# Optimization experiments

Measured on AMD Instinct MI355X. Metric: run time of the kernel, lower is better.

## Reference

```python
import jax, jax.numpy as jnp
import numpy as np

D_MODEL = 1024
NUM_HEADS = 4
EXPAND_K = 1.0
EXPAND_V = 2.0
KEY_DIM = int(D_MODEL * EXPAND_K)      # 1024
VALUE_DIM = int(D_MODEL * EXPAND_V)    # 2048
HEAD_K = KEY_DIM // NUM_HEADS          # 256
HEAD_V = VALUE_DIM // NUM_HEADS        # 512
CHUNK = 64
EPS = 1e-5
ROPE_BASE = 10000.0


def setup_inputs() -> dict:
    key = jax.random.key(0)
    ks = jax.random.split(key, 7)
    B, T = 4, 2048
    s = 0.02
    return {
        "x": jax.random.normal(ks[0], (B, T, D_MODEL), dtype=jnp.float32),
        "Wq": jax.random.normal(ks[1], (KEY_DIM, D_MODEL), dtype=jnp.float32) * s,
        "Wk": jax.random.normal(ks[2], (KEY_DIM, D_MODEL), dtype=jnp.float32) * s,
        "Wv": jax.random.normal(ks[3], (VALUE_DIM, D_MODEL), dtype=jnp.float32) * s,
        "Wg": jax.random.normal(ks[4], (VALUE_DIM, D_MODEL), dtype=jnp.float32) * s,
        "Wo": jax.random.normal(ks[5], (D_MODEL, VALUE_DIM), dtype=jnp.float32) * s,
        "gnorm_w": jnp.ones((HEAD_V,), dtype=jnp.float32),
    }


def _apply_rotary(q, k):
    # q,k: [B,T,H,dk]; NeoX-style (non-interleaved) rotary on full head dim
    d = q.shape[-1]
    half = d // 2
    inv_freq = 1.0 / (ROPE_BASE ** (jnp.arange(0, d, 2, dtype=jnp.float32) / d))
    t = jnp.arange(q.shape[1], dtype=jnp.float32)
    freqs = t[:, None] * inv_freq[None, :]          # [T, d/2]
    cos = jnp.cos(freqs)[None, :, None, :]
    sin = jnp.sin(freqs)[None, :, None, :]

    def rot(x):
        x1, x2 = x[..., :half], x[..., half:]
        return jnp.concatenate([x1 * cos - x2 * sin, x2 * cos + x1 * sin], axis=-1)

    return rot(q), rot(k)


def _chunk_retention(q, k, v, gamma):
    # q,k: [B,T,H,dk]; v: [B,T,H,dv]; gamma: [H] per-head decay
    B, T, H, dk = q.shape
    dv = v.shape[-1]
    C = CHUNK
    N = T // C
    qc = q.reshape(B, N, C, H, dk).transpose(1, 0, 3, 2, 4)  # [N,B,H,C,dk]
    kc = k.reshape(B, N, C, H, dk).transpose(1, 0, 3, 2, 4)
    vc = v.reshape(B, N, C, H, dv).transpose(1, 0, 3, 2, 4)  # [N,B,H,C,dv]

    i = jnp.arange(C, dtype=jnp.float32)
    cross_dec = gamma[:, None] ** (i + 1.0)          # [H,C] gamma^{i+1}: query decay vs incoming state
    k_dec = gamma[:, None] ** (C - 1.0 - i)          # [H,C] key decay toward chunk end
    diff = i[:, None] - i[None, :]                   # [C,C]
    mask = jnp.where(diff >= 0, gamma[:, None, None] ** diff, 0.0)  # [H,C,C]
    gC = gamma ** C                                  # [H]

    def step(S, inp):
        # S: [B,H,dk,dv]
        qb, kb, vb = inp
        attn = jnp.einsum('bhid,bhjd->bhij', qb, kb) * mask
        o_intra = jnp.einsum('bhij,bhjv->bhiv', attn, vb)
        o_inter = jnp.einsum('bhid,bhdv->bhiv', qb * cross_dec[:, :, None], S)
        S_new = gC[:, None, None] * S + jnp.einsum('bhjd,bhjv->bhdv', kb * k_dec[:, :, None], vb)
        return S_new, o_intra + o_inter

    S0 = jnp.zeros((B, H, dk, dv), dtype=q.dtype)
    _, o = jax.lax.scan(step, S0, (qc, kc, vc))      # o: [N,B,H,C,dv]
    return o.transpose(1, 0, 3, 2, 4).reshape(B, T, H, dv)


def reference(x, Wq, Wk, Wv, Wg, Wo, gnorm_w):
    B, T, _ = x.shape
    H = NUM_HEADS
    q = (x @ Wq.T).reshape(B, T, H, HEAD_K)
    k = (x @ Wk.T).reshape(B, T, H, HEAD_K)
    v = (x @ Wv.T).reshape(B, T, H, HEAD_V)
    g = (x @ Wg.T).reshape(B, T, H, HEAD_V)

    q, k = _apply_rotary(q, k)
    q = q * (HEAD_K ** -0.5)

    # fixed multi-scale decays: gamma_h = 1 - 2^{-5-h}
    gamma = 1.0 - jnp.exp2(-5.0 - jnp.arange(H, dtype=jnp.float32))

    o = _chunk_retention(q, k, v, gamma)             # [B,T,H,dv]

    # per-head RMSNorm + swish gate, then output projection
    var = jnp.mean(o * o, axis=-1, keepdims=True)
    o = o * jax.lax.rsqrt(var + EPS) * gnorm_w
    o = o * (g * jax.nn.sigmoid(g))
    return o.reshape(B, T, H * HEAD_V) @ Wo.T
```

## Files before the change

kernel.cpp:

```cpp
#include <hip/hip_runtime.h>
#include <cstdint>
#include <cstddef>

#define T_SEQ 2048
#define DM    1024
#define HK    256
#define HV    512
#define NH    4
#define KDIM  1024
#define VDIM  2048

typedef __attribute__((ext_vector_type(8))) short bf16x8;
typedef __attribute__((ext_vector_type(4))) float f32x4;
#define AS1 __attribute__((address_space(1)))
#define AS3 __attribute__((address_space(3)))

static __device__ inline unsigned short f2bf(float f) {
  unsigned u = __float_as_uint(f);
  unsigned rnd = 0x7fffu + ((u >> 16) & 1u);
  return (unsigned short)((u + rnd) >> 16);
}
static __device__ inline float bf2f(unsigned short h) {
  unsigned u = ((unsigned)h) << 16;
  return __uint_as_float(u);
}

__global__ __launch_bounds__(256) void cast_split(const float* __restrict__ in,
                                                  unsigned short* __restrict__ hi,
                                                  unsigned short* __restrict__ lo,
                                                  int n4) {
  int i = blockIdx.x * 256 + threadIdx.x;
  if (i >= n4) return;
  float4 v = ((const float4*)in)[i];
  ushort4 h, l;
  h.x = f2bf(v.x); l.x = f2bf(v.x - bf2f(h.x));
  h.y = f2bf(v.y); l.y = f2bf(v.y - bf2f(h.y));
  h.z = f2bf(v.z); l.z = f2bf(v.z - bf2f(h.z));
  h.w = f2bf(v.w); l.w = f2bf(v.w - bf2f(h.w));
  ((ushort4*)hi)[i] = h;
  ((ushort4*)lo)[i] = l;
}

__global__ __launch_bounds__(256) void gemm_bf16s(const unsigned short* __restrict__ Ah,
                                                  const unsigned short* __restrict__ Al,
                                                  const unsigned short* __restrict__ Wh,
                                                  const unsigned short* __restrict__ Wl,
                                                  float* __restrict__ C,
                                                  int M, int N, int K) {
  __shared__ unsigned short AhS[128 * 32];
  __shared__ unsigned short AlS[128 * 32];
  __shared__ unsigned short WhS[128 * 32];
  __shared__ unsigned short WlS[128 * 32];
  const int t = threadIdx.x;
  const int l = t & 63;
  const int w = t >> 6;
  const int bm = blockIdx.y * 128;
  const int bn = blockIdx.x * 128;
  const int wm = (w >> 1) * 64;
  const int wn = (w & 1) * 64;

  f32x4 acc[4][4];
#pragma unroll
  for (int i = 0; i < 4; ++i)
#pragma unroll
    for (int j = 0; j < 4; ++j)
#pragma unroll
      for (int r = 0; r < 4; ++r) acc[i][j][r] = 0.f;

  const int srow = w * 32 + (l >> 2);
  const int scol = (l & 3) * 8;
  const size_t gOffA = (size_t)(bm + srow) * K + scol;
  const size_t gOffW = (size_t)(bn + srow) * K + scol;
  const size_t rowStep = (size_t)16 * K;
  unsigned short* lAh0 = &AhS[(w * 32) * 32];
  unsigned short* lAh1 = &AhS[(w * 32 + 16) * 32];
  unsigned short* lAl0 = &AlS[(w * 32) * 32];
  unsigned short* lAl1 = &AlS[(w * 32 + 16) * 32];
  unsigned short* lWh0 = &WhS[(w * 32) * 32];
  unsigned short* lWh1 = &WhS[(w * 32 + 16) * 32];
  unsigned short* lWl0 = &WlS[(w * 32) * 32];
  unsigned short* lWl1 = &WlS[(w * 32 + 16) * 32];

  for (int k0 = 0; k0 < K; k0 += 32) {
    __syncthreads();
    __builtin_amdgcn_global_load_lds((const AS1 void*)(Ah + gOffA + k0),           (AS3 void*)lAh0, 16, 0, 0);
    __builtin_amdgcn_global_load_lds((const AS1 void*)(Ah + gOffA + rowStep + k0), (AS3 void*)lAh1, 16, 0, 0);
    __builtin_amdgcn_global_load_lds((const AS1 void*)(Al + gOffA + k0),           (AS3 void*)lAl0, 16, 0, 0);
    __builtin_amdgcn_global_load_lds((const AS1 void*)(Al + gOffA + rowStep + k0), (AS3 void*)lAl1, 16, 0, 0);
    __builtin_amdgcn_global_load_lds((const AS1 void*)(Wh + gOffW + k0),           (AS3 void*)lWh0, 16, 0, 0);
    __builtin_amdgcn_global_load_lds((const AS1 void*)(Wh + gOffW + rowStep + k0), (AS3 void*)lWh1, 16, 0, 0);
    __builtin_amdgcn_global_load_lds((const AS1 void*)(Wl + gOffW + k0),           (AS3 void*)lWl0, 16, 0, 0);
    __builtin_amdgcn_global_load_lds((const AS1 void*)(Wl + gOffW + rowStep + k0), (AS3 void*)lWl1, 16, 0, 0);
    __syncthreads();

    bf16x8 ah[4], al[4], bh[4], bl[4];
#pragma unroll
    for (int i = 0; i < 4; ++i) {
      int aoff = (wm + i * 16 + (l & 15)) * 32 + (l >> 4) * 8;
      int boff = (wn + i * 16 + (l & 15)) * 32 + (l >> 4) * 8;
      ah[i] = *(const bf16x8*)&AhS[aoff];
      al[i] = *(const bf16x8*)&AlS[aoff];
      bh[i] = *(const bf16x8*)&WhS[boff];
      bl[i] = *(const bf16x8*)&WlS[boff];
    }
#pragma unroll
    for (int i = 0; i < 4; ++i)
#pragma unroll
      for (int j = 0; j < 4; ++j) {
        acc[i][j] = __builtin_amdgcn_mfma_f32_16x16x32_bf16(ah[i], bh[j], acc[i][j], 0, 0, 0);
        acc[i][j] = __builtin_amdgcn_mfma_f32_16x16x32_bf16(ah[i], bl[j], acc[i][j], 0, 0, 0);
        acc[i][j] = __builtin_amdgcn_mfma_f32_16x16x32_bf16(al[i], bh[j], acc[i][j], 0, 0, 0);
      }
  }

  const int cr = (l >> 4) * 4;
  const int cc = l & 15;
#pragma unroll
  for (int i = 0; i < 4; ++i)
#pragma unroll
    for (int j = 0; j < 4; ++j)
#pragma unroll
      for (int r = 0; r < 4; ++r)
        C[(size_t)(bm + wm + i * 16 + cr + r) * N + (bn + wn + j * 16 + cc)] = acc[i][j][r];
}

__global__ __launch_bounds__(256) void rope_kernel(float* __restrict__ q,
                                                   float* __restrict__ k) {
  int idx = blockIdx.x * 256 + threadIdx.x;
  int f  = idx & 127;
  int h  = (idx >> 7) & 3;
  int tt = (idx >> 9) & 2047;
  int b  = idx >> 20;
  size_t a0 = ((size_t)(b * T_SEQ + tt)) * KDIM + h * HK + f;
  size_t a1 = a0 + 128;
  float invf = powf(10000.0f, -(float)f * (1.0f / 128.0f));
  float ang  = (float)tt * invf;
  float s, c;
  sincosf(ang, &s, &c);
  float q1 = q[a0], q2 = q[a1];
  q[a0] = (q1 * c - q2 * s) * 0.0625f;
  q[a1] = (q2 * c + q1 * s) * 0.0625f;
  float k1 = k[a0], k2 = k[a1];
  k[a0] = k1 * c - k2 * s;
  k[a1] = k2 * c + k1 * s;
}

__global__ __launch_bounds__(256) void retn_intra(const float* __restrict__ q,
                                                  const float* __restrict__ k,
                                                  const float* __restrict__ v,
                                                  float* __restrict__ o) {
  const int n = blockIdx.x, h = blockIdx.y, b = blockIdx.z;
  const int t = threadIdx.x;
  const int t0 = n * 64;
  __shared__ float gpow[65];
  __shared__ __align__(16) float qS[64][68];
  __shared__ __align__(16) float kS[64][68];
  __shared__ __align__(16) float attnS[64][68];
  if (t <= 64) {
    float gamma = 1.0f - exp2f(-5.0f - (float)h);
    gpow[t] = powf(gamma, (float)t);
  }
  const size_t baseQK = (size_t)(b * T_SEQ + t0) * KDIM + h * HK;
  const size_t baseV  = (size_t)(b * T_SEQ + t0) * VDIM + h * HV;
  const int i0 = (t >> 4) * 4;
  const int j0 = (t & 15) * 4;
  float acc[4][4] = {};
  for (int s = 0; s < 4; ++s) {
    __syncthreads();
    __builtin_amdgcn_sched_barrier(0);
#pragma unroll
    for (int r = 0; r < 4; ++r) {
      int idx = t + 256 * r;
      int row = idx >> 4, c4 = (idx & 15) * 4;
      *(float4*)&qS[row][c4] = *(const float4*)&q[baseQK + (size_t)row * KDIM + s * 64 + c4];
      *(float4*)&kS[row][c4] = *(const float4*)&k[baseQK + (size_t)row * KDIM + s * 64 + c4];
    }
    __syncthreads();
    __builtin_amdgcn_sched_barrier(0);
    for (int d = 0; d < 64; d += 4) {
      float4 a0 = *(const float4*)&qS[i0 + 0][d];
      float4 a1 = *(const float4*)&qS[i0 + 1][d];
      float4 a2 = *(const float4*)&qS[i0 + 2][d];
      float4 a3 = *(const float4*)&qS[i0 + 3][d];
      float4 b0 = *(const float4*)&kS[j0 + 0][d];
      float4 b1 = *(const float4*)&kS[j0 + 1][d];
      float4 b2 = *(const float4*)&kS[j0 + 2][d];
      float4 b3 = *(const float4*)&kS[j0 + 3][d];
      acc[0][0]=fmaf(a0.x,b0.x,acc[0][0]); acc[0][0]=fmaf(a0.y,b0.y,acc[0][0]); acc[0][0]=fmaf(a0.z,b0.z,acc[0][0]); acc[0][0]=fmaf(a0.w,b0.w,acc[0][0]);
      acc[0][1]=fmaf(a0.x,b1.x,acc[0][1]); acc[0][1]=fmaf(a0.y,b1.y,acc[0][1]); acc[0][1]=fmaf(a0.z,b1.z,acc[0][1]); acc[0][1]=fmaf(a0.w,b1.w,acc[0][1]);
      acc[0][2]=fmaf(a0.x,b2.x,acc[0][2]); acc[0][2]=fmaf(a0.y,b2.y,acc[0][2]); acc[0][2]=fmaf(a0.z,b2.z,acc[0][2]); acc[0][2]=fmaf(a0.w,b2.w,acc[0][2]);
      acc[0][3]=fmaf(a0.x,b3.x,acc[0][3]); acc[0][3]=fmaf(a0.y,b3.y,acc[0][3]); acc[0][3]=fmaf(a0.z,b3.z,acc[0][3]); acc[0][3]=fmaf(a0.w,b3.w,acc[0][3]);
      acc[1][0]=fmaf(a1.x,b0.x,acc[1][0]); acc[1][0]=fmaf(a1.y,b0.y,acc[1][0]); acc[1][0]=fmaf(a1.z,b0.z,acc[1][0]); acc[1][0]=fmaf(a1.w,b0.w,acc[1][0]);
      acc[1][1]=fmaf(a1.x,b1.x,acc[1][1]); acc[1][1]=fmaf(a1.y,b1.y,acc[1][1]); acc[1][1]=fmaf(a1.z,b1.z,acc[1][1]); acc[1][1]=fmaf(a1.w,b1.w,acc[1][1]);
      acc[1][2]=fmaf(a1.x,b2.x,acc[1][2]); acc[1][2]=fmaf(a1.y,b2.y,acc[1][2]); acc[1][2]=fmaf(a1.z,b2.z,acc[1][2]); acc[1][2]=fmaf(a1.w,b2.w,acc[1][2]);
      acc[1][3]=fmaf(a1.x,b3.x,acc[1][3]); acc[1][3]=fmaf(a1.y,b3.y,acc[1][3]); acc[1][3]=fmaf(a1.z,b3.z,acc[1][3]); acc[1][3]=fmaf(a1.w,b3.w,acc[1][3]);
      acc[2][0]=fmaf(a2.x,b0.x,acc[2][0]); acc[2][0]=fmaf(a2.y,b0.y,acc[2][0]); acc[2][0]=fmaf(a2.z,b0.z,acc[2][0]); acc[2][0]=fmaf(a2.w,b0.w,acc[2][0]);
      acc[2][1]=fmaf(a2.x,b1.x,acc[2][1]); acc[2][1]=fmaf(a2.y,b1.y,acc[2][1]); acc[2][1]=fmaf(a2.z,b1.z,acc[2][1]); acc[2][1]=fmaf(a2.w,b1.w,acc[2][1]);
      acc[2][2]=fmaf(a2.x,b2.x,acc[2][2]); acc[2][2]=fmaf(a2.y,b2.y,acc[2][2]); acc[2][2]=fmaf(a2.z,b2.z,acc[2][2]); acc[2][2]=fmaf(a2.w,b2.w,acc[2][2]);
      acc[2][3]=fmaf(a2.x,b3.x,acc[2][3]); acc[2][3]=fmaf(a2.y,b3.y,acc[2][3]); acc[2][3]=fmaf(a2.z,b3.z,acc[2][3]); acc[2][3]=fmaf(a2.w,b3.w,acc[2][3]);
      acc[3][0]=fmaf(a3.x,b0.x,acc[3][0]); acc[3][0]=fmaf(a3.y,b0.y,acc[3][0]); acc[3][0]=fmaf(a3.z,b0.z,acc[3][0]); acc[3][0]=fmaf(a3.w,b0.w,acc[3][0]);
      acc[3][1]=fmaf(a3.x,b1.x,acc[3][1]); acc[3][1]=fmaf(a3.y,b1.y,acc[3][1]); acc[3][1]=fmaf(a3.z,b1.z,acc[3][1]); acc[3][1]=fmaf(a3.w,b1.w,acc[3][1]);
      acc[3][2]=fmaf(a3.x,b2.x,acc[3][2]); acc[3][2]=fmaf(a3.y,b2.y,acc[3][2]); acc[3][2]=fmaf(a3.z,b2.z,acc[3][2]); acc[3][2]=fmaf(a3.w,b2.w,acc[3][2]);
      acc[3][3]=fmaf(a3.x,b3.x,acc[3][3]); acc[3][3]=fmaf(a3.y,b3.y,acc[3][3]); acc[3][3]=fmaf(a3.z,b3.z,acc[3][3]); acc[3][3]=fmaf(a3.w,b3.w,acc[3][3]);
    }
  }
  __syncthreads();
#pragma unroll
  for (int ii = 0; ii < 4; ++ii)
#pragma unroll
    for (int jj = 0; jj < 4; ++jj) {
      int i = i0 + ii, j = j0 + jj;
      attnS[i][j] = (i >= j) ? acc[ii][jj] * gpow[i - j] : 0.0f;
    }
  float (*vS)[68] = qS;
  for (int vb = 0; vb < 8; ++vb) {
    __syncthreads();
    __builtin_amdgcn_sched_barrier(0);
#pragma unroll
    for (int r = 0; r < 4; ++r) {
      int idx = t + 256 * r;
      int row = idx >> 4, c4 = (idx & 15) * 4;
      *(float4*)&vS[row][c4] = *(const float4*)&v[baseV + (size_t)row * VDIM + vb * 64 + c4];
    }
    __syncthreads();
    __builtin_amdgcn_sched_barrier(0);
    float oa[4][4] = {};
    for (int j = 0; j < 64; j += 4) {
      float4 p0 = *(const float4*)&attnS[i0 + 0][j];
      float4 p1 = *(const float4*)&attnS[i0 + 1][j];
      float4 p2 = *(const float4*)&attnS[i0 + 2][j];
      float4 p3 = *(const float4*)&attnS[i0 + 3][j];
      float4 v0 = *(const float4*)&vS[j + 0][j0];
      float4 v1 = *(const float4*)&vS[j + 1][j0];
      float4 v2 = *(const float4*)&vS[j + 2][j0];
      float4 v3 = *(const float4*)&vS[j + 3][j0];
      oa[0][0]=fmaf(p0.x,v0.x,oa[0][0]); oa[0][0]=fmaf(p0.y,v1.x,oa[0][0]); oa[0][0]=fmaf(p0.z,v2.x,oa[0][0]); oa[0][0]=fmaf(p0.w,v3.x,oa[0][0]);
      oa[0][1]=fmaf(p0.x,v0.y,oa[0][1]); oa[0][1]=fmaf(p0.y,v1.y,oa[0][1]); oa[0][1]=fmaf(p0.z,v2.y,oa[0][1]); oa[0][1]=fmaf(p0.w,v3.y,oa[0][1]);
      oa[0][2]=fmaf(p0.x,v0.z,oa[0][2]); oa[0][2]=fmaf(p0.y,v1.z,oa[0][2]); oa[0][2]=fmaf(p0.z,v2.z,oa[0][2]); oa[0][2]=fmaf(p0.w,v3.z,oa[0][2]);
      oa[0][3]=fmaf(p0.x,v0.w,oa[0][3]); oa[0][3]=fmaf(p0.y,v1.w,oa[0][3]); oa[0][3]=fmaf(p0.z,v2.w,oa[0][3]); oa[0][3]=fmaf(p0.w,v3.w,oa[0][3]);
      oa[1][0]=fmaf(p1.x,v0.x,oa[1][0]); oa[1][0]=fmaf(p1.y,v1.x,oa[1][0]); oa[1][0]=fmaf(p1.z,v2.x,oa[1][0]); oa[1][0]=fmaf(p1.w,v3.x,oa[1][0]);
      oa[1][1]=fmaf(p1.x,v0.y,oa[1][1]); oa[1][1]=fmaf(p1.y,v1.y,oa[1][1]); oa[1][1]=fmaf(p1.z,v2.y,oa[1][1]); oa[1][1]=fmaf(p1.w,v3.y,oa[1][1]);
      oa[1][2]=fmaf(p1.x,v0.z,oa[1][2]); oa[1][2]=fmaf(p1.y,v1.z,oa[1][2]); oa[1][2]=fmaf(p1.z,v2.z,oa[1][2]); oa[1][2]=fmaf(p1.w,v3.z,oa[1][2]);
      oa[1][3]=fmaf(p1.x,v0.w,oa[1][3]); oa[1][3]=fmaf(p1.y,v1.w,oa[1][3]); oa[1][3]=fmaf(p1.z,v2.w,oa[1][3]); oa[1][3]=fmaf(p1.w,v3.w,oa[1][3]);
      oa[2][0]=fmaf(p2.x,v0.x,oa[2][0]); oa[2][0]=fmaf(p2.y,v1.x,oa[2][0]); oa[2][0]=fmaf(p2.z,v2.x,oa[2][0]); oa[2][0]=fmaf(p2.w,v3.x,oa[2][0]);
      oa[2][1]=fmaf(p2.x,v0.y,oa[2][1]); oa[2][1]=fmaf(p2.y,v1.y,oa[2][1]); oa[2][1]=fmaf(p2.z,v2.y,oa[2][1]); oa[2][1]=fmaf(p2.w,v3.y,oa[2][1]);
      oa[2][2]=fmaf(p2.x,v0.z,oa[2][2]); oa[2][2]=fmaf(p2.y,v1.z,oa[2][2]); oa[2][2]=fmaf(p2.z,v2.z,oa[2][2]); oa[2][2]=fmaf(p2.w,v3.z,oa[2][2]);
      oa[2][3]=fmaf(p2.x,v0.w,oa[2][3]); oa[2][3]=fmaf(p2.y,v1.w,oa[2][3]); oa[2][3]=fmaf(p2.z,v2.w,oa[2][3]); oa[2][3]=fmaf(p2.w,v3.w,oa[2][3]);
      oa[3][0]=fmaf(p3.x,v0.x,oa[3][0]); oa[3][0]=fmaf(p3.y,v1.x,oa[3][0]); oa[3][0]=fmaf(p3.z,v2.x,oa[3][0]); oa[3][0]=fmaf(p3.w,v3.x,oa[3][0]);
      oa[3][1]=fmaf(p3.x,v0.y,oa[3][1]); oa[3][1]=fmaf(p3.y,v1.y,oa[3][1]); oa[3][1]=fmaf(p3.z,v2.y,oa[3][1]); oa[3][1]=fmaf(p3.w,v3.y,oa[3][1]);
      oa[3][2]=fmaf(p3.x,v0.z,oa[3][2]); oa[3][2]=fmaf(p3.y,v1.z,oa[3][2]); oa[3][2]=fmaf(p3.z,v2.z,oa[3][2]); oa[3][2]=fmaf(p3.w,v3.z,oa[3][2]);
      oa[3][3]=fmaf(p3.x,v0.w,oa[3][3]); oa[3][3]=fmaf(p3.y,v1.w,oa[3][3]); oa[3][3]=fmaf(p3.z,v2.w,oa[3][3]); oa[3][3]=fmaf(p3.w,v3.w,oa[3][3]);
    }
#pragma unroll
    for (int ii = 0; ii < 4; ++ii)
      *(float4*)&o[baseV + (size_t)(i0 + ii) * VDIM + vb * 64 + j0] =
          make_float4(oa[ii][0], oa[ii][1], oa[ii][2], oa[ii][3]);
  }
}


__global__ __launch_bounds__(256) void retn_gstate(const float* __restrict__ k,
                                                   const float* __restrict__ v,
                                                   float* __restrict__ Tbuf) {
  const int bh = blockIdx.x; const int b = bh >> 2, h = bh & 3;
  const int g = blockIdx.y;
  const int dkt = blockIdx.z >> 3, dvt = blockIdx.z & 7;
  const int t = threadIdx.x;
  __shared__ float gpow[65];
  __shared__ __align__(16) float kS[64][68];
  __shared__ __align__(16) float vS[64][68];
  if (t <= 64) gpow[t] = powf(1.0f - exp2f(-5.0f - (float)h), (float)t);
  __syncthreads();
  const float gC = gpow[64];
  const size_t baseK = (size_t)(b * T_SEQ + g * 512) * KDIM + h * HK + dkt * 64;
  const size_t baseV = (size_t)(b * T_SEQ + g * 512) * VDIM + h * HV + dvt * 64;
  const int dk0 = (t & 15) * 4, c0 = (t >> 4) * 4;
  float S[4][4] = {};
  for (int c = 0; c < 8; ++c) {
    const int t0 = c * 64;
    __syncthreads();
    __builtin_amdgcn_sched_barrier(0);
#pragma unroll
    for (int r = 0; r < 4; ++r) {
      int idx = t + 256 * r; int row = idx >> 4, c4 = (idx & 15) * 4;
      float4 kv = *(const float4*)&k[baseK + (size_t)(t0 + row) * KDIM + c4];
      float kd = gpow[63 - row];
      kv.x *= kd; kv.y *= kd; kv.z *= kd; kv.w *= kd;
      *(float4*)&kS[row][c4] = kv;
      *(float4*)&vS[row][c4] = *(const float4*)&v[baseV + (size_t)(t0 + row) * VDIM + c4];
    }
    __syncthreads();
    __builtin_amdgcn_sched_barrier(0);
#pragma unroll
    for (int ii = 0; ii < 4; ++ii)
#pragma unroll
      for (int jj = 0; jj < 4; ++jj) S[ii][jj] *= gC;
    for (int j = 0; j < 64; ++j) {
      float4 kv = *(const float4*)&kS[j][dk0];
      float4 vv = *(const float4*)&vS[j][c0];
      S[0][0] = fmaf(kv.x, vv.x, S[0][0]); S[0][1] = fmaf(kv.x, vv.y, S[0][1]);
      S[0][2] = fmaf(kv.x, vv.z, S[0][2]); S[0][3] = fmaf(kv.x, vv.w, S[0][3]);
      S[1][0] = fmaf(kv.y, vv.x, S[1][0]); S[1][1] = fmaf(kv.y, vv.y, S[1][1]);
      S[1][2] = fmaf(kv.y, vv.z, S[1][2]); S[1][3] = fmaf(kv.y, vv.w, S[1][3]);
      S[2][0] = fmaf(kv.z, vv.x, S[2][0]); S[2][1] = fmaf(kv.z, vv.y, S[2][1]);
      S[2][2] = fmaf(kv.z, vv.z, S[2][2]); S[2][3] = fmaf(kv.z, vv.w, S[2][3]);
      S[3][0] = fmaf(kv.w, vv.x, S[3][0]); S[3][1] = fmaf(kv.w, vv.y, S[3][1]);
      S[3][2] = fmaf(kv.w, vv.z, S[3][2]); S[3][3] = fmaf(kv.w, vv.w, S[3][3]);
    }
  }
  const size_t tb = (((size_t)g * 16 + bh) * 256 + dkt * 64 + dk0) * 512 + (size_t)dvt * 64 + c0;
#pragma unroll
  for (int ii = 0; ii < 4; ++ii)
    *(float4*)&Tbuf[tb + (size_t)ii * 512] = make_float4(S[ii][0], S[ii][1], S[ii][2], S[ii][3]);
}

__global__ __launch_bounds__(256) void retn_scan(float* __restrict__ Tbuf) {
  int i = blockIdx.x * 256 + threadIdx.x;
  int h = (i >> 15) & 3;
  float gamma = 1.0f - exp2f(-5.0f - (float)h);
  float gG = powf(gamma, 512.0f);
  float4* T = (float4*)Tbuf;
  const int slab = 524288;
  float4 t0 = T[i], t1 = T[i + slab], t2 = T[i + 2 * slab];
  float4 s2, s3;
  s2.x = fmaf(gG, t0.x, t1.x); s2.y = fmaf(gG, t0.y, t1.y);
  s2.z = fmaf(gG, t0.z, t1.z); s2.w = fmaf(gG, t0.w, t1.w);
  s3.x = fmaf(gG, s2.x, t2.x); s3.y = fmaf(gG, s2.y, t2.y);
  s3.z = fmaf(gG, s2.z, t2.z); s3.w = fmaf(gG, s2.w, t2.w);
  T[i + slab] = s2; T[i + 2 * slab] = s3;
}

__global__ __launch_bounds__(256) void retn_inter2(const float* __restrict__ q,
                                                   const float* __restrict__ k,
                                                   const float* __restrict__ v,
                                                   float* __restrict__ o,
                                                   const float* __restrict__ Sbuf) {
  const int bh = blockIdx.x; const int b = bh >> 2, h = bh & 3;
  const int g = blockIdx.y;
  const int dvt = blockIdx.z;
  const int t = threadIdx.x;
  __shared__ float gpow[65];
  __shared__ __align__(16) float qS[64][68];
  __shared__ __align__(16) float kS[64][68];
  __shared__ __align__(16) float sS[64][68];
  __shared__ __align__(16) float vS[64][68];
  if (t <= 64) gpow[t] = powf(1.0f - exp2f(-5.0f - (float)h), (float)t);
  __syncthreads();
  const float gC = gpow[64];
  const int rq = (t & 15) * 4;
  const int c0 = (t >> 4) * 4;
  const int i0 = (t >> 4) * 4;
  const int v0 = (t & 15) * 4;
  const size_t baseQK = (size_t)(b * T_SEQ + g * 512) * KDIM + h * HK;
  const size_t baseV  = (size_t)(b * T_SEQ + g * 512) * VDIM + h * HV + (size_t)dvt * 64;

  float S[4][4][4];
  if (g > 0) {
    const size_t sb = (((size_t)(g - 1) * 16 + bh) * 256) * 512 + (size_t)dvt * 64 + c0;
#pragma unroll
    for (int b4 = 0; b4 < 4; ++b4)
#pragma unroll
      for (int i = 0; i < 4; ++i) {
        float4 tmp = *(const float4*)&Sbuf[sb + (size_t)(b4 * 64 + rq + i) * 512];
        S[b4][i][0] = tmp.x; S[b4][i][1] = tmp.y; S[b4][i][2] = tmp.z; S[b4][i][3] = tmp.w;
      }
  } else {
#pragma unroll
    for (int b4 = 0; b4 < 4; ++b4)
#pragma unroll
      for (int i = 0; i < 4; ++i) {
        S[b4][i][0] = 0.f; S[b4][i][1] = 0.f; S[b4][i][2] = 0.f; S[b4][i][3] = 0.f;
      }
  }

  for (int c = 0; c < 8; ++c) {
    const int t0 = c * 64;
    __syncthreads();
    __builtin_amdgcn_sched_barrier(0);
#pragma unroll
    for (int r = 0; r < 4; ++r) {
      int idx = t + 256 * r; int row = idx >> 4, c4 = (idx & 15) * 4;
      *(float4*)&vS[row][c4] = *(const float4*)&v[baseV + (size_t)(t0 + row) * VDIM + c4];
    }
    float oa[4][4] = {};
#pragma unroll
    for (int b4 = 0; b4 < 4; ++b4) {
      __syncthreads();
      __builtin_amdgcn_sched_barrier(0);
#pragma unroll
      for (int i = 0; i < 4; ++i)
        *(float4*)&sS[rq + i][c0] =
            make_float4(S[b4][i][0], S[b4][i][1], S[b4][i][2], S[b4][i][3]);
#pragma unroll
      for (int r = 0; r < 4; ++r) {
        int idx = t + 256 * r; int row = idx >> 4, c4 = (idx & 15) * 4;
        float4 qv = *(const float4*)&q[baseQK + (size_t)(t0 + row) * KDIM + b4 * 64 + c4];
        float gp = gpow[row + 1];
        qv.x *= gp; qv.y *= gp; qv.z *= gp; qv.w *= gp;
        *(float4*)&qS[row][c4] = qv;
      }
#pragma unroll
      for (int r = 0; r < 4; ++r) {
        int idx = t + 256 * r; int row = idx >> 4, c4 = (idx & 15) * 4;
        float4 kv = *(const float4*)&k[baseQK + (size_t)(t0 + row) * KDIM + b4 * 64 + c4];
        float kd = gpow[63 - row];
        kv.x *= kd; kv.y *= kd; kv.z *= kd; kv.w *= kd;
        *(float4*)&kS[row][c4] = kv;
      }
      __syncthreads();
      __builtin_amdgcn_sched_barrier(0);
      for (int d = 0; d < 64; d += 4) {
        float4 a0 = *(const float4*)&qS[i0 + 0][d];
        float4 a1 = *(const float4*)&qS[i0 + 1][d];
        float4 a2 = *(const float4*)&qS[i0 + 2][d];
        float4 a3 = *(const float4*)&qS[i0 + 3][d];
        float4 s0 = *(const float4*)&sS[d + 0][v0];
        float4 s1 = *(const float4*)&sS[d + 1][v0];
        float4 s2 = *(const float4*)&sS[d + 2][v0];
        float4 s3 = *(const float4*)&sS[d + 3][v0];
        oa[0][0]=fmaf(a0.x,s0.x,oa[0][0]); oa[0][0]=fmaf(a0.y,s1.x,oa[0][0]); oa[0][0]=fmaf(a0.z,s2.x,oa[0][0]); oa[0][0]=fmaf(a0.w,s3.x,oa[0][0]);
        oa[0][1]=fmaf(a0.x,s0.y,oa[0][1]); oa[0][1]=fmaf(a0.y,s1.y,oa[0][1]); oa[0][1]=fmaf(a0.z,s2.y,oa[0][1]); oa[0][1]=fmaf(a0.w,s3.y,oa[0][1]);
        oa[0][2]=fmaf(a0.x,s0.z,oa[0][2]); oa[0][2]=fmaf(a0.y,s1.z,oa[0][2]); oa[0][2]=fmaf(a0.z,s2.z,oa[0][2]); oa[0][2]=fmaf(a0.w,s3.z,oa[0][2]);
        oa[0][3]=fmaf(a0.x,s0.w,oa[0][3]); oa[0][3]=fmaf(a0.y,s1.w,oa[0][3]); oa[0][3]=fmaf(a0.z,s2.w,oa[0][3]); oa[0][3]=fmaf(a0.w,s3.w,oa[0][3]);
        oa[1][0]=fmaf(a1.x,s0.x,oa[1][0]); oa[1][0]=fmaf(a1.y,s1.x,oa[1][0]); oa[1][0]=fmaf(a1.z,s2.x,oa[1][0]); oa[1][0]=fmaf(a1.w,s3.x,oa[1][0]);
        oa[1][1]=fmaf(a1.x,s0.y,oa[1][1]); oa[1][1]=fmaf(a1.y,s1.y,oa[1][1]); oa[1][1]=fmaf(a1.z,s2.y,oa[1][1]); oa[1][1]=fmaf(a1.w,s3.y,oa[1][1]);
        oa[1][2]=fmaf(a1.x,s0.z,oa[1][2]); oa[1][2]=fmaf(a1.y,s1.z,oa[1][2]); oa[1][2]=fmaf(a1.z,s2.z,oa[1][2]); oa[1][2]=fmaf(a1.w,s3.z,oa[1][2]);
        oa[1][3]=fmaf(a1.x,s0.w,oa[1][3]); oa[1][3]=fmaf(a1.y,s1.w,oa[1][3]); oa[1][3]=fmaf(a1.z,s2.w,oa[1][3]); oa[1][3]=fmaf(a1.w,s3.w,oa[1][3]);
        oa[2][0]=fmaf(a2.x,s0.x,oa[2][0]); oa[2][0]=fmaf(a2.y,s1.x,oa[2][0]); oa[2][0]=fmaf(a2.z,s2.x,oa[2][0]); oa[2][0]=fmaf(a2.w,s3.x,oa[2][0]);
        oa[2][1]=fmaf(a2.x,s0.y,oa[2][1]); oa[2][1]=fmaf(a2.y,s1.y,oa[2][1]); oa[2][1]=fmaf(a2.z,s2.y,oa[2][1]); oa[2][1]=fmaf(a2.w,s3.y,oa[2][1]);
        oa[2][2]=fmaf(a2.x,s0.z,oa[2][2]); oa[2][2]=fmaf(a2.y,s1.z,oa[2][2]); oa[2][2]=fmaf(a2.z,s2.z,oa[2][2]); oa[2][2]=fmaf(a2.w,s3.z,oa[2][2]);
        oa[2][3]=fmaf(a2.x,s0.w,oa[2][3]); oa[2][3]=fmaf(a2.y,s1.w,oa[2][3]); oa[2][3]=fmaf(a2.z,s2.w,oa[2][3]); oa[2][3]=fmaf(a2.w,s3.w,oa[2][3]);
        oa[3][0]=fmaf(a3.x,s0.x,oa[3][0]); oa[3][0]=fmaf(a3.y,s1.x,oa[3][0]); oa[3][0]=fmaf(a3.z,s2.x,oa[3][0]); oa[3][0]=fmaf(a3.w,s3.x,oa[3][0]);
        oa[3][1]=fmaf(a3.x,s0.y,oa[3][1]); oa[3][1]=fmaf(a3.y,s1.y,oa[3][1]); oa[3][1]=fmaf(a3.z,s2.y,oa[3][1]); oa[3][1]=fmaf(a3.w,s3.y,oa[3][1]);
        oa[3][2]=fmaf(a3.x,s0.z,oa[3][2]); oa[3][2]=fmaf(a3.y,s1.z,oa[3][2]); oa[3][2]=fmaf(a3.z,s2.z,oa[3][2]); oa[3][2]=fmaf(a3.w,s3.z,oa[3][2]);
        oa[3][3]=fmaf(a3.x,s0.w,oa[3][3]); oa[3][3]=fmaf(a3.y,s1.w,oa[3][3]); oa[3][3]=fmaf(a3.z,s2.w,oa[3][3]); oa[3][3]=fmaf(a3.w,s3.w,oa[3][3]);
      }
#pragma unroll
      for (int ii = 0; ii < 4; ++ii) {
        S[b4][ii][0] *= gC; S[b4][ii][1] *= gC; S[b4][ii][2] *= gC; S[b4][ii][3] *= gC;
      }
      for (int j = 0; j < 64; ++j) {
        float4 kv = *(const float4*)&kS[j][rq];
        float4 vv = *(const float4*)&vS[j][c0];
        S[b4][0][0] = fmaf(kv.x, vv.x, S[b4][0][0]); S[b4][0][1] = fmaf(kv.x, vv.y, S[b4][0][1]);
        S[b4][0][2] = fmaf(kv.x, vv.z, S[b4][0][2]); S[b4][0][3] = fmaf(kv.x, vv.w, S[b4][0][3]);
        S[b4][1][0] = fmaf(kv.y, vv.x, S[b4][1][0]); S[b4][1][1] = fmaf(kv.y, vv.y, S[b4][1][1]);
        S[b4][1][2] = fmaf(kv.y, vv.z, S[b4][1][2]); S[b4][1][3] = fmaf(kv.y, vv.w, S[b4][1][3]);
        S[b4][2][0] = fmaf(kv.z, vv.x, S[b4][2][0]); S[b4][2][1] = fmaf(kv.z, vv.y, S[b4][2][1]);
        S[b4][2][2] = fmaf(kv.z, vv.z, S[b4][2][2]); S[b4][2][3] = fmaf(kv.z, vv.w, S[b4][2][3]);
        S[b4][3][0] = fmaf(kv.w, vv.x, S[b4][3][0]); S[b4][3][1] = fmaf(kv.w, vv.y, S[b4][3][1]);
        S[b4][3][2] = fmaf(kv.w, vv.z, S[b4][3][2]); S[b4][3][3] = fmaf(kv.w, vv.w, S[b4][3][3]);
      }
    }
#pragma unroll
    for (int ii = 0; ii < 4; ++ii) {
      size_t addr = baseV + (size_t)(t0 + i0 + ii) * VDIM + v0;
      float4 ov = *(const float4*)&o[addr];
      ov.x += oa[ii][0]; ov.y += oa[ii][1]; ov.z += oa[ii][2]; ov.w += oa[ii][3];
      *(float4*)&o[addr] = ov;
    }
  }
}

__global__ __launch_bounds__(256) void norm_gate(float* __restrict__ o,
                                                 const float* __restrict__ g,
                                                 const float* __restrict__ gnw) {
  const int row = blockIdx.x;
  const size_t base = (size_t)row * 512;
  const int t = threadIdx.x;
  float x0 = o[base + t], x1 = o[base + t + 256];
  float ss = x0 * x0 + x1 * x1;
#pragma unroll
  for (int off = 32; off > 0; off >>= 1) ss += __shfl_down(ss, off, 64);
  __shared__ float wsum[4];
  if ((t & 63) == 0) wsum[t >> 6] = ss;
  __syncthreads();
  float tot = wsum[0] + wsum[1] + wsum[2] + wsum[3];
  float scale = rsqrtf(tot * (1.0f / 512.0f) + 1e-5f);
  float g0 = g[base + t], g1 = g[base + t + 256];
  o[base + t]       = x0 * scale * gnw[t]       * (g0 / (1.0f + expf(-g0)));
  o[base + t + 256] = x1 * scale * gnw[t + 256] * (g1 / (1.0f + expf(-g1)));
}

extern "C" void kernel_launch(void* const* d_in, const int* in_sizes, int n_in,
                              void* d_out, int out_size, void* d_ws, size_t ws_size,
                              hipStream_t stream) {
  const float* x   = (const float*)d_in[0];
  const float* Wq  = (const float*)d_in[1];
  const float* Wk  = (const float*)d_in[2];
  const float* Wv  = (const float*)d_in[3];
  const float* Wg  = (const float*)d_in[4];
  const float* Wo  = (const float*)d_in[5];
  const float* gnw = (const float*)d_in[6];
  float* out = (float*)d_out;

  const size_t M8 = (size_t)8192;
  float* q  = (float*)d_ws;
  float* kk = q  + M8 * 1024;
  float* v  = kk + M8 * 1024;
  float* o  = v  + M8 * 2048;
  unsigned short* xh  = (unsigned short*)(o + M8 * 2048);
  unsigned short* xl  = xh  + M8 * 1024;
  unsigned short* wqh = xl  + M8 * 1024;
  unsigned short* wql = wqh + (size_t)1024 * 1024;
  unsigned short* wkh = wql + (size_t)1024 * 1024;
  unsigned short* wkl = wkh + (size_t)1024 * 1024;
  unsigned short* wvh = wkl + (size_t)1024 * 1024;
  unsigned short* wvl = wvh + (size_t)2048 * 1024;
  unsigned short* wgh = wvl + (size_t)2048 * 1024;
  unsigned short* wgl = wgh + (size_t)2048 * 1024;
  unsigned short* woh = wgl + (size_t)2048 * 1024;
  unsigned short* wol = woh + (size_t)2048 * 1024;
  unsigned short* oh  = (unsigned short*)v;
  unsigned short* ol  = oh + M8 * 2048;
  float* g = q;
  float* Tbuf = (float*)d_out;

  dim3 blk(256);
  cast_split<<<dim3(8192), blk, 0, stream>>>(x,  xh,  xl,  2097152);
  cast_split<<<dim3(1024), blk, 0, stream>>>(Wq, wqh, wql, 262144);
  cast_split<<<dim3(1024), blk, 0, stream>>>(Wk, wkh, wkl, 262144);
  cast_split<<<dim3(2048), blk, 0, stream>>>(Wv, wvh, wvl, 524288);
  cast_split<<<dim3(2048), blk, 0, stream>>>(Wg, wgh, wgl, 524288);
  cast_split<<<dim3(2048), blk, 0, stream>>>(Wo, woh, wol, 524288);

  gemm_bf16s<<<dim3(8, 64),  blk, 0, stream>>>(xh, xl, wqh, wql, q,  8192, 1024, 1024);
  gemm_bf16s<<<dim3(8, 64),  blk, 0, stream>>>(xh, xl, wkh, wkl, kk, 8192, 1024, 1024);
  gemm_bf16s<<<dim3(16, 64), blk, 0, stream>>>(xh, xl, wvh, wvl, v,  8192, 2048, 1024);
  rope_kernel<<<dim3(16384), blk, 0, stream>>>(q, kk);
  retn_gstate<<<dim3(16, 3, 32), blk, 0, stream>>>(kk, v, Tbuf);
  retn_scan<<<dim3(2048), blk, 0, stream>>>(Tbuf);
  retn_intra<<<dim3(32, 4, 4),  blk, 0, stream>>>(q, kk, v, o);
  retn_inter2<<<dim3(16, 4, 8), blk, 0, stream>>>(q, kk, v, o, Tbuf);
  gemm_bf16s<<<dim3(16, 64), blk, 0, stream>>>(xh, xl, wgh, wgl, g, 8192, 2048, 1024);
  norm_gate<<<dim3(32768), blk, 0, stream>>>(o, g, gnw);
  cast_split<<<dim3(16384), blk, 0, stream>>>(o, oh, ol, 4194304);
  gemm_bf16s<<<dim3(8, 64),  blk, 0, stream>>>(oh, ol, woh, wol, out, 8192, 1024, 2048);
}
```

Measured before the change: 1.026 ms.

## Merge QKV GEMMs, fuse norm-gate with bf16 split, skip zero-state inter work

New measurement: 1.011 ms. No clear change (-1.4%).

```diff
diff --git a/kernel.cpp b/kernel.cpp
--- a/kernel.cpp
+++ b/kernel.cpp
@@ -56,6 +56,100 @@
   const int w = t >> 6;
   const int bm = blockIdx.y * 128;
   const int bn = blockIdx.x * 128;
+  const int wm = (w >> 1) * 64;
+  const int wn = (w & 1) * 64;
+
+  f32x4 acc[4][4];
+#pragma unroll
+  for (int i = 0; i < 4; ++i)
+#pragma unroll
+    for (int j = 0; j < 4; ++j)
+#pragma unroll
+      for (int r = 0; r < 4; ++r) acc[i][j][r] = 0.f;
+
+  const int srow = w * 32 + (l >> 2);
+  const int scol = (l & 3) * 8;
+  const size_t gOffA = (size_t)(bm + srow) * K + scol;
+  const size_t gOffW = (size_t)(bn + srow) * K + scol;
+  const size_t rowStep = (size_t)16 * K;
+  unsigned short* lAh0 = &AhS[(w * 32) * 32];
+  unsigned short* lAh1 = &AhS[(w * 32 + 16) * 32];
+  unsigned short* lAl0 = &AlS[(w * 32) * 32];
+  unsigned short* lAl1 = &AlS[(w * 32 + 16) * 32];
+  unsigned short* lWh0 = &WhS[(w * 32) * 32];
+  unsigned short* lWh1 = &WhS[(w * 32 + 16) * 32];
+  unsigned short* lWl0 = &WlS[(w * 32) * 32];
+  unsigned short* lWl1 = &WlS[(w * 32 + 16) * 32];
+
+  for (int k0 = 0; k0 < K; k0 += 32) {
+    __syncthreads();
+    __builtin_amdgcn_global_load_lds((const AS1 void*)(Ah + gOffA + k0),           (AS3 void*)lAh0, 16, 0, 0);
+    __builtin_amdgcn_global_load_lds((const AS1 void*)(Ah + gOffA + rowStep + k0), (AS3 void*)lAh1, 16, 0, 0);
+    __builtin_amdgcn_global_load_lds((const AS1 void*)(Al + gOffA + k0),           (AS3 void*)lAl0, 16, 0, 0);
+    __builtin_amdgcn_global_load_lds((const AS1 void*)(Al + gOffA + rowStep + k0), (AS3 void*)lAl1, 16, 0, 0);
+    __builtin_amdgcn_global_load_lds((const AS1 void*)(Wh + gOffW + k0),           (AS3 void*)lWh0, 16, 0, 0);
+    __builtin_amdgcn_global_load_lds((const AS1 void*)(Wh + gOffW + rowStep + k0), (AS3 void*)lWh1, 16, 0, 0);
+    __builtin_amdgcn_global_load_lds((const AS1 void*)(Wl + gOffW + k0),           (AS3 void*)lWl0, 16, 0, 0);
+    __builtin_amdgcn_global_load_lds((const AS1 void*)(Wl + gOffW + rowStep + k0), (AS3 void*)lWl1, 16, 0, 0);
+    __syncthreads();
+
+    bf16x8 ah[4], al[4], bh[4], bl[4];
+#pragma unroll
+    for (int i = 0; i < 4; ++i) {
+      int aoff = (wm + i * 16 + (l & 15)) * 32 + (l >> 4) * 8;
+      int boff = (wn + i * 16 + (l & 15)) * 32 + (l >> 4) * 8;
+      ah[i] = *(const bf16x8*)&AhS[aoff];
+      al[i] = *(const bf16x8*)&AlS[aoff];
+      bh[i] = *(const bf16x8*)&WhS[boff];
+      bl[i] = *(const bf16x8*)&WlS[boff];
+    }
+#pragma unroll
+    for (int i = 0; i < 4; ++i)
+#pragma unroll
+      for (int j = 0; j < 4; ++j) {
+        acc[i][j] = __builtin_amdgcn_mfma_f32_16x16x32_bf16(ah[i], bh[j], acc[i][j], 0, 0, 0);
+        acc[i][j] = __builtin_amdgcn_mfma_f32_16x16x32_bf16(ah[i], bl[j], acc[i][j], 0, 0, 0);
+        acc[i][j] = __builtin_amdgcn_mfma_f32_16x16x32_bf16(al[i], bh[j], acc[i][j], 0, 0, 0);
+      }
+  }
+
+  const int cr = (l >> 4) * 4;
+  const int cc = l & 15;
+#pragma unroll
+  for (int i = 0; i < 4; ++i)
+#pragma unroll
+    for (int j = 0; j < 4; ++j)
+#pragma unroll
+      for (int r = 0; r < 4; ++r)
+        C[(size_t)(bm + wm + i * 16 + cr + r) * N + (bn + wn + j * 16 + cc)] = acc[i][j][r];
+}
+
+__global__ __launch_bounds__(256) void gemm_qkv(const unsigned short* __restrict__ Ah,
+                                                const unsigned short* __restrict__ Al,
+                                                const unsigned short* __restrict__ wqh,
+                                                const unsigned short* __restrict__ wql,
+                                                const unsigned short* __restrict__ wkh,
+                                                const unsigned short* __restrict__ wkl,
+                                                const unsigned short* __restrict__ wvh,
+                                                const unsigned short* __restrict__ wvl,
+                                                float* __restrict__ q,
+                                                float* __restrict__ kk,
+                                                float* __restrict__ v) {
+  const int K = 1024;
+  const int bx = blockIdx.x;
+  const unsigned short* Wh; const unsigned short* Wl; float* C; int N; int bn;
+  if (bx < 8)       { Wh = wqh; Wl = wql; C = q;  N = 1024; bn = bx * 128; }
+  else if (bx < 16) { Wh = wkh; Wl = wkl; C = kk; N = 1024; bn = (bx - 8) * 128; }
+  else              { Wh = wvh; Wl = wvl; C = v;  N = 2048; bn = (bx - 16) * 128; }
+
+  __shared__ unsigned short AhS[128 * 32];
+  __shared__ unsigned short AlS[128 * 32];
+  __shared__ unsigned short WhS[128 * 32];
+  __shared__ unsigned short WlS[128 * 32];
+  const int t = threadIdx.x;
+  const int l = t & 63;
+  const int w = t >> 6;
+  const int bm = blockIdx.y * 128;
   const int wm = (w >> 1) * 64;
   const int wn = (w & 1) * 64;
 
@@ -375,6 +469,7 @@
 
   for (int c = 0; c < 8; ++c) {
     const int t0 = c * 64;
+    const bool doO = (g > 0 || c > 0);
     __syncthreads();
     __builtin_amdgcn_sched_barrier(0);
 #pragma unroll
@@ -387,17 +482,19 @@
     for (int b4 = 0; b4 < 4; ++b4) {
       __syncthreads();
       __builtin_amdgcn_sched_barrier(0);
-#pragma unroll
-      for (int i = 0; i < 4; ++i)
-        *(float4*)&sS[rq + i][c0] =
-            make_float4(S[b4][i][0], S[b4][i][1], S[b4][i][2], S[b4][i][3]);
-#pragma unroll
-      for (int r = 0; r < 4; ++r) {
-        int idx = t + 256 * r; int row = idx >> 4, c4 = (idx & 15) * 4;
-        float4 qv = *(const float4*)&q[baseQK + (size_t)(t0 + row) * KDIM + b4 * 64 + c4];
-        float gp = gpow[row + 1];
-        qv.x *= gp; qv.y *= gp; qv.z *= gp; qv.w *= gp;
-        *(float4*)&qS[row][c4] = qv;
+      if (doO) {
+#pragma unroll
+        for (int i = 0; i < 4; ++i)
+          *(float4*)&sS[rq + i][c0] =
+              make_float4(S[b4][i][0], S[b4][i][1], S[b4][i][2], S[b4][i][3]);
+#pragma unroll
+        for (int r = 0; r < 4; ++r) {
+          int idx = t + 256 * r; int row = idx >> 4, c4 = (idx & 15) * 4;
+          float4 qv = *(const float4*)&q[baseQK + (size_t)(t0 + row) * KDIM + b4 * 64 + c4];
+          float gp = gpow[row + 1];
+          qv.x *= gp; qv.y *= gp; qv.z *= gp; qv.w *= gp;
+          *(float4*)&qS[row][c4] = qv;
+        }
       }
 #pragma unroll
       for (int r = 0; r < 4; ++r) {
@@ -409,31 +506,33 @@
       }
       __syncthreads();
       __builtin_amdgcn_sched_barrier(0);
-      for (int d = 0; d < 64; d += 4) {
-        float4 a0 = *(const float4*)&qS[i0 + 0][d];
-        float4 a1 = *(const float4*)&qS[i0 + 1][d];
-        float4 a2 = *(const float4*)&qS[i0 + 2][d];
-        float4 a3 = *(const float4*)&qS[i0 + 3][d];
-        float4 s0 = *(const float4*)&sS[d + 0][v0];
-        float4 s1 = *(const float4*)&sS[d + 1][v0];
-        float4 s2 = *(const float4*)&sS[d + 2][v0];
-        float4 s3 = *(const float4*)&sS[d + 3][v0];
-        oa[0][0]=fmaf(a0.x,s0.x,oa[0][0]); oa[0][0]=fmaf(a0.y,s1.x,oa[0][0]); oa[0][0]=fmaf(a0.z,s2.x,oa[0][0]); oa[0][0]=fmaf(a0.w,s3.x,oa[0][0]);
-        oa[0][1]=fmaf(a0.x,s0.y,oa[0][1]); oa[0][1]=fmaf(a0.y,s1.y,oa[0][1]); oa[0][1]=fmaf(a0.z,s2.y,oa[0][1]); oa[0][1]=fmaf(a0.w,s3.y,oa[0][1]);
-        oa[0][2]=fmaf(a0.x,s0.z,oa[0][2]); oa[0][2]=fmaf(a0.y,s1.z,oa[0][2]); oa[0][2]=fmaf(a0.z,s2.z,oa[0][2]); oa[0][2]=fmaf(a0.w,s3.z,oa[0][2]);
-        oa[0][3]=fmaf(a0.x,s0.w,oa[0][3]); oa[0][3]=fmaf(a0.y,s1.w,oa[0][3]); oa[0][3]=fmaf(a0.z,s2.w,oa[0][3]); oa[0][3]=fmaf(a0.w,s3.w,oa[0][3]);
-        oa[1][0]=fmaf(a1.x,s0.x,oa[1][0]); oa[1][0]=fmaf(a1.y,s1.x,oa[1][0]); oa[1][0]=fmaf(a1.z,s2.x,oa[1][0]); oa[1][0]=fmaf(a1.w,s3.x,oa[1][0]);
-        oa[1][1]=fmaf(a1.x,s0.y,oa[1][1]); oa[1][1]=fmaf(a1.y,s1.y,oa[1][1]); oa[1][1]=fmaf(a1.z,s2.y,oa[1][1]); oa[1][1]=fmaf(a1.w,s3.y,oa[1][1]);
-        oa[1][2]=fmaf(a1.x,s0.z,oa[1][2]); oa[1][2]=fmaf(a1.y,s1.z,oa[1][2]); oa[1][2]=fmaf(a1.z,s2.z,oa[1][2]); oa[1][2]=fmaf(a1.w,s3.z,oa[1][2]);
-        oa[1][3]=fmaf(a1.x,s0.w,oa[1][3]); oa[1][3]=fmaf(a1.y,s1.w,oa[1][3]); oa[1][3]=fmaf(a1.z,s2.w,oa[1][3]); oa[1][3]=fmaf(a1.w,s3.w,oa[1][3]);
-        oa[2][0]=fmaf(a2.x,s0.x,oa[2][0]); oa[2][0]=fmaf(a2.y,s1.x,oa[2][0]); oa[2][0]=fmaf(a2.z,s2.x,oa[2][0]); oa[2][0]=fmaf(a2.w,s3.x,oa[2][0]);
-        oa[2][1]=fmaf(a2.x,s0.y,oa[2][1]); oa[2][1]=fmaf(a2.y,s1.y,oa[2][1]); oa[2][1]=fmaf(a2.z,s2.y,oa[2][1]); oa[2][1]=fmaf(a2.w,s3.y,oa[2][1]);
-        oa[2][2]=fmaf(a2.x,s0.z,oa[2][2]); oa[2][2]=fmaf(a2.y,s1.z,oa[2][2]); oa[2][2]=fmaf(a2.z,s2.z,oa[2][2]); oa[2][2]=fmaf(a2.w,s3.z,oa[2][2]);
-        oa[2][3]=fmaf(a2.x,s0.w,oa[2][3]); oa[2][3]=fmaf(a2.y,s1.w,oa[2][3]); oa[2][3]=fmaf(a2.z,s2.w,oa[2][3]); oa[2][3]=fmaf(a2.w,s3.w,oa[2][3]);
-        oa[3][0]=fmaf(a3.x,s0.x,oa[3][0]); oa[3][0]=fmaf(a3.y,s1.x,oa[3][0]); oa[3][0]=fmaf(a3.z,s2.x,oa[3][0]); oa[3][0]=fmaf(a3.w,s3.x,oa[3][0]);
-        oa[3][1]=fmaf(a3.x,s0.y,oa[3][1]); oa[3][1]=fmaf(a3.y,s1.y,oa[3][1]); oa[3][1]=fmaf(a3.z,s2.y,oa[3][1]); oa[3][1]=fmaf(a3.w,s3.y,oa[3][1]);
-        oa[3][2]=fmaf(a3.x,s0.z,oa[3][2]); oa[3][2]=fmaf(a3.y,s1.z,oa[3][2]); oa[3][2]=fmaf(a3.z,s2.z,oa[3][2]); oa[3][2]=fmaf(a3.w,s3.z,oa[3][2]);
-        oa[3][3]=fmaf(a3.x,s0.w,oa[3][3]); oa[3][3]=fmaf(a3.y,s1.w,oa[3][3]); oa[3][3]=fmaf(a3.z,s2.w,oa[3][3]); oa[3][3]=fmaf(a3.w,s3.w,oa[3][3]);
+      if (doO) {
+        for (int d = 0; d < 64; d += 4) {
+          float4 a0 = *(const float4*)&qS[i0 + 0][d];
+          float4 a1 = *(const float4*)&qS[i0 + 1][d];
+          float4 a2 = *(const float4*)&qS[i0 + 2][d];
+          float4 a3 = *(const float4*)&qS[i0 + 3][d];
+          float4 s0 = *(const float4*)&sS[d + 0][v0];
+          float4 s1 = *(const float4*)&sS[d + 1][v0];
+          float4 s2 = *(const float4*)&sS[d + 2][v0];
+          float4 s3 = *(const float4*)&sS[d + 3][v0];
+          oa[0][0]=fmaf(a0.x,s0.x,oa[0][0]); oa[0][0]=fmaf(a0.y,s1.x,oa[0][0]); oa[0][0]=fmaf(a0.z,s2.x,oa[0][0]); oa[0][0]=fmaf(a0.w,s3.x,oa[0][0]);
+          oa[0][1]=fmaf(a0.x,s0.y,oa[0][1]); oa[0][1]=fmaf(a0.y,s1.y,oa[0][1]); oa[0][1]=fmaf(a0.z,s2.y,oa[0][1]); oa[0][1]=fmaf(a0.w,s3.y,oa[0][1]);
+          oa[0][2]=fmaf(a0.x,s0.z,oa[0][2]); oa[0][2]=fmaf(a0.y,s1.z,oa[0][2]); oa[0][2]=fmaf(a0.z,s2.z,oa[0][2]); oa[0][2]=fmaf(a0.w,s3.z,oa[0][2]);
+          oa[0][3]=fmaf(a0.x,s0.w,oa[0][3]); oa[0][3]=fmaf(a0.y,s1.w,oa[0][3]); oa[0][3]=fmaf(a0.z,s2.w,oa[0][3]); oa[0][3]=fmaf(a0.w,s3.w,oa[0][3]);
+          oa[1][0]=fmaf(a1.x,s0.x,oa[1][0]); oa[1][0]=fmaf(a1.y,s1.x,oa[1][0]); oa[1][0]=fmaf(a1.z,s2.x,oa[1][0]); oa[1][0]=fmaf(a1.w,s3.x,oa[1][0]);
+          oa[1][1]=fmaf(a1.x,s0.y,oa[1][1]); oa[1][1]=fmaf(a1.y,s1.y,oa[1][1]); oa[1][1]=fmaf(a1.z,s2.y,oa[1][1]); oa[1][1]=fmaf(a1.w,s3.y,oa[1][1]);
+          oa[1][2]=fmaf(a1.x,s0.z,oa[1][2]); oa[1][2]=fmaf(a1.y,s1.z,oa[1][2]); oa[1][2]=fmaf(a1.z,s2.z,oa[1][2]); oa[1][2]=fmaf(a1.w,s3.z,oa[1][2]);
+          oa[1][3]=fmaf(a1.x,s0.w,oa[1][3]); oa[1][3]=fmaf(a1.y,s1.w,oa[1][3]); oa[1][3]=fmaf(a1.z,s2.w,oa[1][3]); oa[1][3]=fmaf(a1.w,s3.w,oa[1][3]);
+          oa[2][0]=fmaf(a2.x,s0.x,oa[2][0]); oa[2][0]=fmaf(a2.y,s1.x,oa[2][0]); oa[2][0]=fmaf(a2.z,s2.x,oa[2][0]); oa[2][0]=fmaf(a2.w,s3.x,oa[2][0]);
+          oa[2][1]=fmaf(a2.x,s0.y,oa[2][1]); oa[2][1]=fmaf(a2.y,s1.y,oa[2][1]); oa[2][1]=fmaf(a2.z,s2.y,oa[2][1]); oa[2][1]=fmaf(a2.w,s3.y,oa[2][1]);
+          oa[2][2]=fmaf(a2.x,s0.z,oa[2][2]); oa[2][2]=fmaf(a2.y,s1.z,oa[2][2]); oa[2][2]=fmaf(a2.z,s2.z,oa[2][2]); oa[2][2]=fmaf(a2.w,s3.z,oa[2][2]);
+          oa[2][3]=fmaf(a2.x,s0.w,oa[2][3]); oa[2][3]=fmaf(a2.y,s1.w,oa[2][3]); oa[2][3]=fmaf(a2.z,s2.w,oa[2][3]); oa[2][3]=fmaf(a2.w,s3.w,oa[2][3]);
+          oa[3][0]=fmaf(a3.x,s0.x,oa[3][0]); oa[3][0]=fmaf(a3.y,s1.x,oa[3][0]); oa[3][0]=fmaf(a3.z,s2.x,oa[3][0]); oa[3][0]=fmaf(a3.w,s3.x,oa[3][0]);
+          oa[3][1]=fmaf(a3.x,s0.y,oa[3][1]); oa[3][1]=fmaf(a3.y,s1.y,oa[3][1]); oa[3][1]=fmaf(a3.z,s2.y,oa[3][1]); oa[3][1]=fmaf(a3.w,s3.y,oa[3][1]);
+          oa[3][2]=fmaf(a3.x,s0.z,oa[3][2]); oa[3][2]=fmaf(a3.y,s1.z,oa[3][2]); oa[3][2]=fmaf(a3.z,s2.z,oa[3][2]); oa[3][2]=fmaf(a3.w,s3.z,oa[3][2]);
+          oa[3][3]=fmaf(a3.x,s0.w,oa[3][3]); oa[3][3]=fmaf(a3.y,s1.w,oa[3][3]); oa[3][3]=fmaf(a3.z,s2.w,oa[3][3]); oa[3][3]=fmaf(a3.w,s3.w,oa[3][3]);
+        }
       }
 #pragma unroll
       for (int ii = 0; ii < 4; ++ii) {
@@ -452,19 +551,23 @@
         S[b4][3][2] = fmaf(kv.w, vv.z, S[b4][3][2]); S[b4][3][3] = fmaf(kv.w, vv.w, S[b4][3][3]);
       }
     }
-#pragma unroll
-    for (int ii = 0; ii < 4; ++ii) {
-      size_t addr = baseV + (size_t)(t0 + i0 + ii) * VDIM + v0;
-      float4 ov = *(const float4*)&o[addr];
-      ov.x += oa[ii][0]; ov.y += oa[ii][1]; ov.z += oa[ii][2]; ov.w += oa[ii][3];
-      *(float4*)&o[addr] = ov;
-    }
-  }
-}
-
-__global__ __launch_bounds__(256) void norm_gate(float* __restrict__ o,
-                                                 const float* __restrict__ g,
-                                                 const float* __restrict__ gnw) {
+    if (doO) {
+#pragma unroll
+      for (int ii = 0; ii < 4; ++ii) {
+        size_t addr = baseV + (size_t)(t0 + i0 + ii) * VDIM + v0;
+        float4 ov = *(const float4*)&o[addr];
+        ov.x += oa[ii][0]; ov.y += oa[ii][1]; ov.z += oa[ii][2]; ov.w += oa[ii][3];
+        *(float4*)&o[addr] = ov;
+      }
+    }
+  }
+}
+
+__global__ __launch_bounds__(256) void norm_gate_cast(const float* __restrict__ o,
+                                                      const float* __restrict__ g,
+                                                      const float* __restrict__ gnw,
+                                                      unsigned short* __restrict__ oh,
+                                                      unsigned short* __restrict__ ol) {
   const int row = blockIdx.x;
   const size_t base = (size_t)row * 512;
   const int t = threadIdx.x;
@@ -478,8 +581,12 @@
   float tot = wsum[0] + wsum[1] + wsum[2] + wsum[3];
   float scale = rsqrtf(tot * (1.0f / 512.0f) + 1e-5f);
   float g0 = g[base + t], g1 = g[base + t + 256];
-  o[base + t]       = x0 * scale * gnw[t]       * (g0 / (1.0f + expf(-g0)));
-  o[base + t + 256] = x1 * scale * gnw[t + 256] * (g1 / (1.0f + expf(-g1)));
+  float r0 = x0 * scale * gnw[t]       * (g0 / (1.0f + expf(-g0)));
+  float r1 = x1 * scale * gnw[t + 256] * (g1 / (1.0f + expf(-g1)));
+  unsigned short h0 = f2bf(r0);
+  unsigned short h1 = f2bf(r1);
+  oh[base + t]       = h0; ol[base + t]       = f2bf(r0 - bf2f(h0));
+  oh[base + t + 256] = h1; ol[base + t + 256] = f2bf(r1 - bf2f(h1));
 }
 
 extern "C" void kernel_launch(void* const* d_in, const int* in_sizes, int n_in,
@@ -524,16 +631,13 @@
   cast_split<<<dim3(2048), blk, 0, stream>>>(Wg, wgh, wgl, 524288);
   cast_split<<<dim3(2048), blk, 0, stream>>>(Wo, woh, wol, 524288);
 
-  gemm_bf16s<<<dim3(8, 64),  blk, 0, stream>>>(xh, xl, wqh, wql, q,  8192, 1024, 1024);
-  gemm_bf16s<<<dim3(8, 64),  blk, 0, stream>>>(xh, xl, wkh, wkl, kk, 8192, 1024, 1024);
-  gemm_bf16s<<<dim3(16, 64), blk, 0, stream>>>(xh, xl, wvh, wvl, v,  8192, 2048, 1024);
+  gemm_qkv<<<dim3(32, 64), blk, 0, stream>>>(xh, xl, wqh, wql, wkh, wkl, wvh, wvl, q, kk, v);
   rope_kernel<<<dim3(16384), blk, 0, stream>>>(q, kk);
   retn_gstate<<<dim3(16, 3, 32), blk, 0, stream>>>(kk, v, Tbuf);
   retn_scan<<<dim3(2048), blk, 0, stream>>>(Tbuf);
   retn_intra<<<dim3(32, 4, 4),  blk, 0, stream>>>(q, kk, v, o);
   retn_inter2<<<dim3(16, 4, 8), blk, 0, stream>>>(q, kk, v, o, Tbuf);
   gemm_bf16s<<<dim3(16, 64), blk, 0, stream>>>(xh, xl, wgh, wgl, g, 8192, 2048, 1024);
-  norm_gate<<<dim3(32768), blk, 0, stream>>>(o, g, gnw);
-  cast_split<<<dim3(16384), blk, 0, stream>>>(o, oh, ol, 4194304);
+  norm_gate_cast<<<dim3(32768), blk, 0, stream>>>(o, g, gnw, oh, ol);
   gemm_bf16s<<<dim3(8, 64),  blk, 0, stream>>>(oh, ol, woh, wol, out, 8192, 1024, 2048);
 }
```
